# Performance work log

Hardware: AMD Instinct MI355X
Metric: run time of the kernel (lower is better)

Reference implementation:

```python
import jax, jax.numpy as jnp
import numpy as np

N_ENT = 15000  # entity id range; also used for relation ids in this synthetic setup

def _triple_key(h, r, t):
    # Unique int64 key per (h, r, t) triple; max ~15000^3 < 2^63.
    return (h * N_ENT + r) * N_ENT + t

def setup_inputs() -> dict:
    key = jax.random.key(0)
    k1, k2, k3, k4 = jax.random.split(key, 4)
    Q, N = 100000, 10000000
    heads = jax.random.randint(k1, (Q,), 0, N_ENT, dtype=jnp.int64)
    rels = jax.random.randint(k2, (Q,), 0, N_ENT, dtype=jnp.int64)
    tails = jax.random.randint(k3, (Q,), 0, N_ENT, dtype=jnp.int64)
    data = jax.random.randint(k4, (3, N), 0, N_ENT, dtype=jnp.int64)
    return {"heads": heads, "rels": rels, "tails": tails, "data": data}

def reference(heads, rels, tails, data) -> jnp.ndarray:
    # Faithful to PerfeCT.forward: response[i] = 1 iff (heads[i], rels[i], tails[i])
    # appears as a row of data.T; output = 10 * (response - 0.5).
    data_keys = jnp.sort(_triple_key(data[0], data[1], data[2]))  # [N]
    q_keys = _triple_key(heads, rels, tails)                       # [Q]
    idx = jnp.searchsorted(data_keys, q_keys)
    idx = jnp.clip(idx, 0, data_keys.shape[0] - 1)
    member = (data_keys[idx] == q_keys).astype(jnp.float32)        # [Q]
    return 10.0 * (member - 0.5)
```

## Files before the change

### kernel.cpp

```cpp
#include <hip/hip_runtime.h>
#include <stdint.h>


typedef int iv4 __attribute__((ext_vector_type(4)));

#define EMPTY  0xFFFFFFFFu
#define BWORDS 32768
#define QSLOTS 6
#define TPB    1024

static __device__ __forceinline__ uint32_t mix32(uint32_t x) {
    x ^= x >> 16; x *= 0x85ebca6bu;
    x ^= x >> 13; x *= 0xc2b2ae35u;
    x ^= x >> 16;
    return x;
}
static __device__ __forceinline__ uint32_t hash2(uint32_t x) {
    return mix32(x ^ 0x9E3779B9u);
}
static __device__ __forceinline__ uint32_t key32(int h, int r, int t) {
    return ((uint32_t)h * 15000u + (uint32_t)r) * 15000u + (uint32_t)t;
}
static __device__ __forceinline__ void bloom_wm(uint32_t key, uint32_t* w, uint32_t* m) {
    uint32_t z = mix32(key);
    *w = z & (BWORDS - 1u);
    *m = (1u << ((z >> 15) & 31u)) | (1u << ((z >> 20) & 31u));
}

__global__ void k_zero(uint32_t* __restrict__ p, int zeroWords, int totalWords) {
    int stride = gridDim.x * blockDim.x;
    for (int i = blockIdx.x * blockDim.x + threadIdx.x; i < totalWords; i += stride)
        p[i] = (i < zeroWords) ? 0u : EMPTY;
}

__global__ void k_insert(const int* __restrict__ qh, const int* __restrict__ qr,
                         const int* __restrict__ qt,
                         uint32_t* __restrict__ bloom, uint32_t* __restrict__ keys,
                         uint32_t tmask, int Q) {
    int i = blockIdx.x * blockDim.x + threadIdx.x;
    if (i >= Q) return;
    uint32_t key = key32(qh[i], qr[i], qt[i]);
    if (key == EMPTY) return;
    uint32_t w, m; bloom_wm(key, &w, &m);
    atomicOr(&bloom[w], m);
    uint32_t slot = hash2(key) & tmask;
    while (true) {
        uint32_t prev = atomicCAS(&keys[slot], EMPTY, key);
        if (prev == EMPTY || prev == key) return;
        slot = (slot + 1) & tmask;
    }
}

static __device__ __forceinline__ void probe_mark(uint32_t key,
                                                  const uint32_t* __restrict__ keys,
                                                  uint32_t* __restrict__ flagbits,
                                                  uint32_t tmask) {
    uint32_t slot = hash2(key) & tmask;
    while (true) {
        uint32_t v = keys[slot];
        if (v == key) { atomicOr(&flagbits[slot >> 5], 1u << (slot & 31)); return; }
        if (v == EMPTY) return;
        slot = (slot + 1) & tmask;
    }
}

static __device__ __forceinline__ void ovf_push(uint32_t key,
                                                uint32_t* __restrict__ ovf_cnt,
                                                uint32_t* __restrict__ ovf, uint32_t ovfcap,
                                                const uint32_t* __restrict__ keys,
                                                uint32_t* __restrict__ flagbits, uint32_t tmask) {
    uint32_t idx = atomicAdd(ovf_cnt, 1u);
    if (idx < ovfcap) ovf[idx] = key;
    else probe_mark(key, keys, flagbits, tmask);
}

__global__ __launch_bounds__(TPB) void k_scan(
        const int* __restrict__ dh, const int* __restrict__ dr,
        const int* __restrict__ dt,
        const uint32_t* __restrict__ bloom,
        const uint32_t* __restrict__ keys,
        uint32_t* __restrict__ flagbits, uint32_t* __restrict__ sent,
        uint32_t* __restrict__ ovf_cnt, uint32_t* __restrict__ ovf, uint32_t ovfcap,
        uint32_t tmask, int noct, int N) {
    __shared__ uint32_t lb[BWORDS];
    __shared__ uint32_t qb[TPB * QSLOTS];
    for (int i = threadIdx.x; i < BWORDS; i += TPB) lb[i] = bloom[i];
    __syncthreads();

    const iv4* H = (const iv4*)dh;
    const iv4* R = (const iv4*)dr;
    const iv4* T = (const iv4*)dt;
    int cnt = 0;
    int stride = gridDim.x * blockDim.x;

#define TESTQ(kk, vv, mm)                                                          \
    if ((kk) == EMPTY) *sent = 1u;                                                 \
    else if (((vv) & (mm)) == (mm)) {                                              \
        if (cnt < QSLOTS) qb[cnt * TPB + threadIdx.x] = (kk);                      \
        else ovf_push((kk), ovf_cnt, ovf, ovfcap, keys, flagbits, tmask);          \
        cnt++;                                                                     \
    }

    for (int j = blockIdx.x * blockDim.x + threadIdx.x; j < noct; j += stride) {
        iv4 hA = H[j], rA = R[j], tA = T[j];
        iv4 hB = H[j + noct], rB = R[j + noct], tB = T[j + noct];
        uint32_t k0 = key32(hA.x, rA.x, tA.x), k1 = key32(hA.y, rA.y, tA.y);
        uint32_t k2 = key32(hA.z, rA.z, tA.z), k3 = key32(hA.w, rA.w, tA.w);
        uint32_t k4 = key32(hB.x, rB.x, tB.x), k5 = key32(hB.y, rB.y, tB.y);
        uint32_t k6 = key32(hB.z, rB.z, tB.z), k7 = key32(hB.w, rB.w, tB.w);
        uint32_t w0,m0,w1,m1,w2,m2,w3,m3,w4,m4,w5,m5,w6,m6,w7,m7;
        bloom_wm(k0,&w0,&m0); bloom_wm(k1,&w1,&m1); bloom_wm(k2,&w2,&m2); bloom_wm(k3,&w3,&m3);
        bloom_wm(k4,&w4,&m4); bloom_wm(k5,&w5,&m5); bloom_wm(k6,&w6,&m6); bloom_wm(k7,&w7,&m7);
        uint32_t v0 = lb[w0], v1 = lb[w1], v2 = lb[w2], v3 = lb[w3];
        uint32_t v4 = lb[w4], v5 = lb[w5], v6 = lb[w6], v7 = lb[w7];
        TESTQ(k0, v0, m0) TESTQ(k1, v1, m1) TESTQ(k2, v2, m2) TESTQ(k3, v3, m3)
        TESTQ(k4, v4, m4) TESTQ(k5, v5, m5) TESTQ(k6, v6, m6) TESTQ(k7, v7, m7)
    }
#undef TESTQ

    int rem = N - 8 * noct;
    if (blockIdx.x == 0 && (int)threadIdx.x < rem) {
        int j = 8 * noct + threadIdx.x;
        uint32_t k = key32(dh[j], dr[j], dt[j]);
        if (k == EMPTY) *sent = 1u;
        else probe_mark(k, keys, flagbits, tmask);
    }

    int m = cnt < QSLOTS ? cnt : QSLOTS;
    for (int c = 0; c < m; ++c)
        probe_mark(qb[c * TPB + threadIdx.x], keys, flagbits, tmask);
}

__global__ void k_probe(const uint32_t* __restrict__ ovf,
                        const uint32_t* __restrict__ ovf_cnt, uint32_t ovfcap,
                        const uint32_t* __restrict__ keys,
                        uint32_t* __restrict__ flagbits, uint32_t tmask) {
    uint32_t n = *ovf_cnt; if (n > ovfcap) n = ovfcap;
    int stride = gridDim.x * blockDim.x;
    for (uint32_t i = blockIdx.x * blockDim.x + threadIdx.x; i < n; i += stride)
        probe_mark(ovf[i], keys, flagbits, tmask);
}

__global__ void k_out(const int* __restrict__ qh, const int* __restrict__ qr,
                      const int* __restrict__ qt,
                      const uint32_t* __restrict__ keys,
                      const uint32_t* __restrict__ flagbits,
                      const uint32_t* __restrict__ sent,
                      float* __restrict__ out, uint32_t tmask, int Q) {
    int i = blockIdx.x * blockDim.x + threadIdx.x;
    if (i >= Q) return;
    uint32_t key = key32(qh[i], qr[i], qt[i]);
    float v = -5.0f;
    if (key == EMPTY) {
        v = (*sent) ? 5.0f : -5.0f;
    } else {
        uint32_t slot = hash2(key) & tmask;
        while (true) {
            uint32_t kv = keys[slot];
            if (kv == key) { v = ((flagbits[slot >> 5] >> (slot & 31)) & 1u) ? 5.0f : -5.0f; break; }
            if (kv == EMPTY) break;
            slot = (slot + 1) & tmask;
        }
    }
    out[i] = v;
}

extern "C" void kernel_launch(void* const* d_in, const int* in_sizes, int n_in,
                              void* d_out, int out_size, void* d_ws, size_t ws_size,
                              hipStream_t stream) {
    const int* qh = (const int*)d_in[0];
    const int* qr = (const int*)d_in[1];
    const int* qt = (const int*)d_in[2];
    const int* data = (const int*)d_in[3];
    int Q = in_sizes[0];
    int N = in_sizes[3] / 3;
    const int* dh = data;
    const int* dr = data + (size_t)N;
    const int* dt = data + 2 * (size_t)N;
    float* out = (float*)d_out;

    int tb = 18;
    uint32_t ovfcap = 65536;
    size_t bloomB = (size_t)BWORDS * 4;
    size_t need = bloomB + ((size_t)1 << (tb - 3)) + 256 + ((size_t)4 << tb) + 4ull * ovfcap;
    if (need > ws_size) { ovfcap = 8192;
        need = bloomB + ((size_t)1 << (tb - 3)) + 256 + ((size_t)4 << tb) + 4ull * ovfcap; }
    if (need > ws_size) { tb = 17; }
    size_t flagB = (size_t)1 << (tb - 3);
    uint32_t tmask = ((uint32_t)1 << tb) - 1u;

    uint32_t* bloom    = (uint32_t*)d_ws;
    uint32_t* flagbits = (uint32_t*)((char*)d_ws + bloomB);
    uint32_t* hdr      = (uint32_t*)((char*)d_ws + bloomB + flagB);
    uint32_t* keys     = (uint32_t*)((char*)d_ws + bloomB + flagB + 256);
    uint32_t* ovf      = (uint32_t*)((char*)d_ws + bloomB + flagB + 256 + ((size_t)4 << tb));

    int zeroWords  = (int)((bloomB + flagB + 256) / 4);
    int totalWords = zeroWords + (1 << tb);
    k_zero<<<1024, 256, 0, stream>>>((uint32_t*)d_ws, zeroWords, totalWords);

    int qblocks = (Q + 255) / 256;
    k_insert<<<qblocks, 256, 0, stream>>>(qh, qr, qt, bloom, keys, tmask, Q);

    int noct = N / 8;
    k_scan<<<256, TPB, 0, stream>>>(dh, dr, dt, bloom, keys, flagbits,
                                    hdr, hdr + 1, ovf, ovfcap, tmask, noct, N);

    k_probe<<<64, 256, 0, stream>>>(ovf, hdr + 1, ovfcap, keys, flagbits, tmask);

    k_out<<<qblocks, 256, 0, stream>>>(qh, qr, qt, keys, flagbits, hdr, out, tmask, Q);
}
```

Measured before the change: 220.0 us.

## Drop overflow buffer and probe kernel, widen scan to 16 keys per thread

Removes the global overflow queue and the separate k_probe launch; when the per-thread shared queue is full, keys that pass the Bloom filter are probed inline. The scan loop now loads four int4 groups per array (16 triples per iteration) instead of two, and the Bloom filter is copied to LDS with vector loads. This cuts one kernel launch and the global atomic counter traffic, and adds more loads in flight per thread. In exchange, register pressure rises and inline probing can cause divergence when many candidates pass the filter.

```diff
diff --git a/kernel.cpp b/kernel.cpp
--- a/kernel.cpp
+++ b/kernel.cpp
@@ -64,27 +64,20 @@
     }
 }
 
-static __device__ __forceinline__ void ovf_push(uint32_t key,
-                                                uint32_t* __restrict__ ovf_cnt,
-                                                uint32_t* __restrict__ ovf, uint32_t ovfcap,
-                                                const uint32_t* __restrict__ keys,
-                                                uint32_t* __restrict__ flagbits, uint32_t tmask) {
-    uint32_t idx = atomicAdd(ovf_cnt, 1u);
-    if (idx < ovfcap) ovf[idx] = key;
-    else probe_mark(key, keys, flagbits, tmask);
-}
-
 __global__ __launch_bounds__(TPB) void k_scan(
         const int* __restrict__ dh, const int* __restrict__ dr,
         const int* __restrict__ dt,
         const uint32_t* __restrict__ bloom,
         const uint32_t* __restrict__ keys,
         uint32_t* __restrict__ flagbits, uint32_t* __restrict__ sent,
-        uint32_t* __restrict__ ovf_cnt, uint32_t* __restrict__ ovf, uint32_t ovfcap,
-        uint32_t tmask, int noct, int N) {
+        uint32_t tmask, int nhex, int N) {
     __shared__ uint32_t lb[BWORDS];
     __shared__ uint32_t qb[TPB * QSLOTS];
-    for (int i = threadIdx.x; i < BWORDS; i += TPB) lb[i] = bloom[i];
+    {
+        const iv4* gb = (const iv4*)bloom;
+        iv4* lb4 = (iv4*)lb;
+        for (int i = threadIdx.x; i < BWORDS / 4; i += TPB) lb4[i] = gb[i];
+    }
     __syncthreads();
 
     const iv4* H = (const iv4*)dh;
@@ -96,31 +89,32 @@
 #define TESTQ(kk, vv, mm)                                                          \
     if ((kk) == EMPTY) *sent = 1u;                                                 \
     else if (((vv) & (mm)) == (mm)) {                                              \
-        if (cnt < QSLOTS) qb[cnt * TPB + threadIdx.x] = (kk);                      \
-        else ovf_push((kk), ovf_cnt, ovf, ovfcap, keys, flagbits, tmask);          \
-        cnt++;                                                                     \
+        if (cnt < QSLOTS) { qb[cnt * TPB + threadIdx.x] = (kk); cnt++; }           \
+        else probe_mark((kk), keys, flagbits, tmask);                              \
+    }
+#define GRP4(h4, r4, t4)                                                           \
+    {                                                                              \
+        uint32_t k0 = key32((h4).x, (r4).x, (t4).x), k1 = key32((h4).y, (r4).y, (t4).y); \
+        uint32_t k2 = key32((h4).z, (r4).z, (t4).z), k3 = key32((h4).w, (r4).w, (t4).w); \
+        uint32_t w0,m0,w1,m1,w2,m2,w3,m3;                                          \
+        bloom_wm(k0,&w0,&m0); bloom_wm(k1,&w1,&m1);                                \
+        bloom_wm(k2,&w2,&m2); bloom_wm(k3,&w3,&m3);                                \
+        uint32_t v0 = lb[w0], v1 = lb[w1], v2 = lb[w2], v3 = lb[w3];               \
+        TESTQ(k0, v0, m0) TESTQ(k1, v1, m1) TESTQ(k2, v2, m2) TESTQ(k3, v3, m3)    \
     }
 
-    for (int j = blockIdx.x * blockDim.x + threadIdx.x; j < noct; j += stride) {
-        iv4 hA = H[j], rA = R[j], tA = T[j];
-        iv4 hB = H[j + noct], rB = R[j + noct], tB = T[j + noct];
-        uint32_t k0 = key32(hA.x, rA.x, tA.x), k1 = key32(hA.y, rA.y, tA.y);
-        uint32_t k2 = key32(hA.z, rA.z, tA.z), k3 = key32(hA.w, rA.w, tA.w);
-        uint32_t k4 = key32(hB.x, rB.x, tB.x), k5 = key32(hB.y, rB.y, tB.y);
-        uint32_t k6 = key32(hB.z, rB.z, tB.z), k7 = key32(hB.w, rB.w, tB.w);
-        uint32_t w0,m0,w1,m1,w2,m2,w3,m3,w4,m4,w5,m5,w6,m6,w7,m7;
-        bloom_wm(k0,&w0,&m0); bloom_wm(k1,&w1,&m1); bloom_wm(k2,&w2,&m2); bloom_wm(k3,&w3,&m3);
-        bloom_wm(k4,&w4,&m4); bloom_wm(k5,&w5,&m5); bloom_wm(k6,&w6,&m6); bloom_wm(k7,&w7,&m7);
-        uint32_t v0 = lb[w0], v1 = lb[w1], v2 = lb[w2], v3 = lb[w3];
-        uint32_t v4 = lb[w4], v5 = lb[w5], v6 = lb[w6], v7 = lb[w7];
-        TESTQ(k0, v0, m0) TESTQ(k1, v1, m1) TESTQ(k2, v2, m2) TESTQ(k3, v3, m3)
-        TESTQ(k4, v4, m4) TESTQ(k5, v5, m5) TESTQ(k6, v6, m6) TESTQ(k7, v7, m7)
+    for (int j = blockIdx.x * blockDim.x + threadIdx.x; j < nhex; j += stride) {
+        iv4 hA = H[j], hB = H[j + nhex], hC = H[j + 2 * nhex], hD = H[j + 3 * nhex];
+        iv4 rA = R[j], rB = R[j + nhex], rC = R[j + 2 * nhex], rD = R[j + 3 * nhex];
+        iv4 tA = T[j], tB = T[j + nhex], tC = T[j + 2 * nhex], tD = T[j + 3 * nhex];
+        GRP4(hA, rA, tA) GRP4(hB, rB, tB) GRP4(hC, rC, tC) GRP4(hD, rD, tD)
     }
+#undef GRP4
 #undef TESTQ
 
-    int rem = N - 8 * noct;
+    int rem = N - 16 * nhex;
     if (blockIdx.x == 0 && (int)threadIdx.x < rem) {
-        int j = 8 * noct + threadIdx.x;
+        int j = 16 * nhex + threadIdx.x;
         uint32_t k = key32(dh[j], dr[j], dt[j]);
         if (k == EMPTY) *sent = 1u;
         else probe_mark(k, keys, flagbits, tmask);
@@ -129,16 +123,6 @@
     int m = cnt < QSLOTS ? cnt : QSLOTS;
     for (int c = 0; c < m; ++c)
         probe_mark(qb[c * TPB + threadIdx.x], keys, flagbits, tmask);
-}
-
-__global__ void k_probe(const uint32_t* __restrict__ ovf,
-                        const uint32_t* __restrict__ ovf_cnt, uint32_t ovfcap,
-                        const uint32_t* __restrict__ keys,
-                        uint32_t* __restrict__ flagbits, uint32_t tmask) {
-    uint32_t n = *ovf_cnt; if (n > ovfcap) n = ovfcap;
-    int stride = gridDim.x * blockDim.x;
-    for (uint32_t i = blockIdx.x * blockDim.x + threadIdx.x; i < n; i += stride)
-        probe_mark(ovf[i], keys, flagbits, tmask);
 }
 
 __global__ void k_out(const int* __restrict__ qh, const int* __restrict__ qr,
@@ -180,12 +164,9 @@
     float* out = (float*)d_out;
 
     int tb = 18;
-    uint32_t ovfcap = 65536;
     size_t bloomB = (size_t)BWORDS * 4;
-    size_t need = bloomB + ((size_t)1 << (tb - 3)) + 256 + ((size_t)4 << tb) + 4ull * ovfcap;
-    if (need > ws_size) { ovfcap = 8192;
-        need = bloomB + ((size_t)1 << (tb - 3)) + 256 + ((size_t)4 << tb) + 4ull * ovfcap; }
-    if (need > ws_size) { tb = 17; }
+    size_t need = bloomB + ((size_t)1 << (tb - 3)) + 256 + ((size_t)4 << tb);
+    if (need > ws_size) tb = 17;
     size_t flagB = (size_t)1 << (tb - 3);
     uint32_t tmask = ((uint32_t)1 << tb) - 1u;
 
@@ -193,7 +174,6 @@
     uint32_t* flagbits = (uint32_t*)((char*)d_ws + bloomB);
     uint32_t* hdr      = (uint32_t*)((char*)d_ws + bloomB + flagB);
     uint32_t* keys     = (uint32_t*)((char*)d_ws + bloomB + flagB + 256);
-    uint32_t* ovf      = (uint32_t*)((char*)d_ws + bloomB + flagB + 256 + ((size_t)4 << tb));
 
     int zeroWords  = (int)((bloomB + flagB + 256) / 4);
     int totalWords = zeroWords + (1 << tb);
@@ -202,11 +182,9 @@
     int qblocks = (Q + 255) / 256;
     k_insert<<<qblocks, 256, 0, stream>>>(qh, qr, qt, bloom, keys, tmask, Q);
 
-    int noct = N / 8;
+    int nhex = N / 16;
     k_scan<<<256, TPB, 0, stream>>>(dh, dr, dt, bloom, keys, flagbits,
-                                    hdr, hdr + 1, ovf, ovfcap, tmask, noct, N);
-
-    k_probe<<<64, 256, 0, stream>>>(ovf, hdr + 1, ovfcap, keys, flagbits, tmask);
+                                    hdr, tmask, nhex, N);
 
     k_out<<<qblocks, 256, 0, stream>>>(qh, qr, qt, keys, flagbits, hdr, out, tmask, Q);
 }
```

New measurement: 222.0 us. No clear change (+0.9%).
